# Optimization experiments

Measured on AMD Instinct MI355X. Metric: run time of the kernel, lower is better.

The kernel has to match this reference:

```python
import jax, jax.numpy as jnp
import numpy as np

B, H, S, D = 4, 8, 8192, 64


def setup_inputs() -> dict:
    key = jax.random.key(0)
    kq, kk, kv_, kqm, kkm = jax.random.split(key, 5)
    q = jax.random.normal(kq, (B, H, S, D), dtype=jnp.float32)
    k = jax.random.normal(kk, (B, H, S, D), dtype=jnp.float32)
    v = jax.random.normal(kv_, (B, H, S, D), dtype=jnp.float32)
    q_mask = jax.random.randint(kqm, (B, S), 0, 2).astype(jnp.bool_)
    kv_mask = jax.random.randint(kkm, (B, S), 0, 2).astype(jnp.bool_)
    return {"q": q, "k": k, "v": v, "q_mask": q_mask, "kv_mask": kv_mask}


def reference(q, k, v, q_mask, kv_mask):
    # Linear (kernelized) attention branch: feature map phi(x) = elu(x) + 1
    qe = jax.nn.elu(q) + 1.0
    ke = jax.nn.elu(k) + 1.0
    qm = q_mask.astype(q.dtype)[:, None, :, None]   # [B,1,S,1]
    km = kv_mask.astype(q.dtype)[:, None, :, None]
    qe = qe * qm
    ke = ke * km
    ve = v * km
    s = v.shape[2]
    # kv: [B,H,D,D] contraction over kv sequence
    kv = jnp.einsum('bhsd,bhsc->bhdc', ke, ve / s)
    # normalizer per query position: [B,H,L]
    div = 1.0 / (jnp.einsum('bhld,bhsd->bhl', qe, ke) + 1e-6)
    out = s * jnp.einsum('bhld,bhdc,bhl->bhlc', qe, kv, div)
    return out
```

## Files before the change

### kernel.cpp

```cpp
#include <hip/hip_runtime.h>


#define S_LEN 8192
#define NBH 32
#define KVSTRIDE 4160
#define NCHUNK 32
#define K3_XB 32

typedef __attribute__((ext_vector_type(4))) float f32x4;

__device__ __forceinline__ float elu1(float x) {
  return x > 0.0f ? (x + 1.0f) : __expf(x);
}

__global__ __launch_bounds__(256, 4) void k1_partial(
    const float* __restrict__ kin, const float* __restrict__ vin,
    const int* __restrict__ kv_mask, float* __restrict__ partials, int seg_rows) {
  __shared__ float ke_lds[64 * 64];
  __shared__ float ve_lds[64 * 64];
  const int tid = threadIdx.x;
  const int seg = blockIdx.x, bh = blockIdx.y, b = bh >> 3;
  const int rbase = seg * seg_rows;
  const int dg = tid >> 4, cg = tid & 15;
  const float* kbase = kin + (size_t)bh * S_LEN * 64;
  const float* vbase = vin + (size_t)bh * S_LEN * 64;
  const int* mbase = kv_mask + b * S_LEN;

  f32x4 kr[4], vr[4];
  float mr[4];
  float acc[4][4];
#pragma unroll
  for (int i = 0; i < 4; ++i)
#pragma unroll
    for (int j = 0; j < 4; ++j) acc[i][j] = 0.f;
  f32x4 ksump = {0.f, 0.f, 0.f, 0.f};

#define LOAD_T(r0_)                                                    \
  {                                                                    \
    const float* kp_ = kbase + (size_t)(r0_) * 64;                     \
    const float* vp_ = vbase + (size_t)(r0_) * 64;                     \
    _Pragma("unroll")                                                  \
    for (int i_ = 0; i_ < 4; ++i_) {                                   \
      int f_ = tid + 256 * i_;                                         \
      kr[i_] = *(const f32x4*)(kp_ + (size_t)f_ * 4);                  \
      vr[i_] = *(const f32x4*)(vp_ + (size_t)f_ * 4);                  \
      mr[i_] = mbase[(r0_) + dg + 16 * i_] ? 1.0f : 0.0f;              \
    }                                                                  \
  }

#define STORE_T()                                                      \
  {                                                                    \
    _Pragma("unroll")                                                  \
    for (int i_ = 0; i_ < 4; ++i_) {                                   \
      int row_ = dg + 16 * i_;                                         \
      float m_ = mr[i_];                                               \
      float mv_ = m_ * (1.0f / 8192.0f);                               \
      f32x4 ke4_, ve4_;                                                \
      _Pragma("unroll")                                                \
      for (int j_ = 0; j_ < 4; ++j_) {                                 \
        ke4_[j_] = elu1(kr[i_][j_]) * m_;                              \
        ve4_[j_] = vr[i_][j_] * mv_;                                   \
      }                                                                \
      ksump += ke4_;                                                   \
      *(f32x4*)&ke_lds[row_ * 64 + cg * 4] = ke4_;                     \
      *(f32x4*)&ve_lds[row_ * 64 + cg * 4] = ve4_;                     \
    }                                                                  \
  }

#define COMPUTE_T()                                                    \
  {                                                                    \
    _Pragma("unroll 4")                                                \
    for (int s_ = 0; s_ < 64; ++s_) {                                  \
      f32x4 kd_ = *(const f32x4*)&ke_lds[s_ * 64 + dg * 4];            \
      f32x4 vc_ = *(const f32x4*)&ve_lds[s_ * 64 + cg * 4];            \
      _Pragma("unroll")                                                \
      for (int i_ = 0; i_ < 4; ++i_)                                   \
        _Pragma("unroll")                                              \
        for (int j_ = 0; j_ < 4; ++j_)                                 \
          acc[i_][j_] = fmaf(kd_[i_], vc_[j_], acc[i_][j_]);           \
    }                                                                  \
  }

  const int ntiles = seg_rows >> 6;
  LOAD_T(rbase)
  for (int t = 0; t < ntiles; ++t) {
    if (t) __syncthreads();
    STORE_T()
    __syncthreads();
    if (t + 1 < ntiles) LOAD_T(rbase + (t + 1) * 64)
    COMPUTE_T()
  }

  float* p = partials + ((size_t)bh * gridDim.x + seg) * KVSTRIDE;
#pragma unroll
  for (int i = 0; i < 4; ++i) {
    f32x4 o;
#pragma unroll
    for (int j = 0; j < 4; ++j) o[j] = acc[i][j];
    *(f32x4*)&p[(dg * 4 + i) * 64 + cg * 4] = o;
  }
  __syncthreads();
  *(f32x4*)&ke_lds[tid * 4] = ksump;
  __syncthreads();
  if (tid < 64) {
    float s = 0.f;
#pragma unroll
    for (int g = 0; g < 16; ++g)
      s += ke_lds[(g * 16 + (tid >> 2)) * 4 + (tid & 3)];
    p[4096 + tid] = s;
  }
#undef LOAD_T
#undef STORE_T
#undef COMPUTE_T
}

__global__ __launch_bounds__(256) void k2_reduce(
    const float* __restrict__ partials, float* __restrict__ kvg, int nchunk) {
  const int idx = blockIdx.x * 256 + threadIdx.x;
  if (idx >= NBH * KVSTRIDE) return;
  const int bh = idx / KVSTRIDE;
  const int e = idx - bh * KVSTRIDE;
  const float* p = partials + (size_t)bh * nchunk * KVSTRIDE + e;
  float s0 = 0.f, s1 = 0.f, s2 = 0.f, s3 = 0.f;
  int c = 0;
  for (; c + 4 <= nchunk; c += 4) {
    s0 += p[(size_t)(c + 0) * KVSTRIDE];
    s1 += p[(size_t)(c + 1) * KVSTRIDE];
    s2 += p[(size_t)(c + 2) * KVSTRIDE];
    s3 += p[(size_t)(c + 3) * KVSTRIDE];
  }
  for (; c < nchunk; ++c) s0 += p[(size_t)c * KVSTRIDE];
  kvg[idx] = (s0 + s1) + (s2 + s3);
}

__global__ __launch_bounds__(256, 4) void k3_out(
    const float* __restrict__ qin, const int* __restrict__ q_mask,
    const float* __restrict__ kvg, float* __restrict__ out) {
  __shared__ float kv_lds[64 * 64];
  __shared__ float qe_lds[64 * 68];
  __shared__ float ks_lds[64];
  const int tid = threadIdx.x;
  const int xb = blockIdx.x, bh = blockIdx.y, b = bh >> 3;
  const int lg = tid >> 4, cg = tid & 15;
  const float* kvb = kvg + (size_t)bh * KVSTRIDE;
  const float* qb = qin + (size_t)bh * S_LEN * 64;
  const int* mb = q_mask + b * S_LEN;

#pragma unroll
  for (int i = 0; i < 4; ++i) {
    int f = tid + 256 * i;
    *(f32x4*)&kv_lds[f * 4] = *(const f32x4*)(kvb + (size_t)f * 4);
  }
  if (tid < 64) ks_lds[tid] = kvb[4096 + tid];

  f32x4 qr[4];
  float mr[4];

#define LOADQ(r0_)                                                     \
  {                                                                    \
    const float* qp_ = qb + (size_t)(r0_) * 64;                        \
    _Pragma("unroll")                                                  \
    for (int i_ = 0; i_ < 4; ++i_) {                                   \
      int f_ = tid + 256 * i_;                                         \
      qr[i_] = *(const f32x4*)(qp_ + (size_t)f_ * 4);                  \
      mr[i_] = mb[(r0_) + lg + 16 * i_] ? 1.0f : 0.0f;                 \
    }                                                                  \
  }

#define STOREQ()                                                       \
  {                                                                    \
    _Pragma("unroll")                                                  \
    for (int i_ = 0; i_ < 4; ++i_) {                                   \
      int row_ = lg + 16 * i_;                                         \
      float m_ = mr[i_];                                               \
      f32x4 qe_;                                                       \
      _Pragma("unroll")                                                \
      for (int j_ = 0; j_ < 4; ++j_) qe_[j_] = elu1(qr[i_][j_]) * m_;  \
      *(f32x4*)&qe_lds[row_ * 68 + cg * 4] = qe_;                      \
    }                                                                  \
  }

  const int c0 = xb * 4;
  LOADQ(c0 * 64)
  for (int t = 0; t < 4; ++t) {
    if (t) __syncthreads();
    STOREQ()
    __syncthreads();
    if (t + 1 < 4) LOADQ((c0 + t + 1) * 64)
    float acc[4][4];
    float den[4];
#pragma unroll
    for (int il = 0; il < 4; ++il) {
      den[il] = 0.f;
#pragma unroll
      for (int j = 0; j < 4; ++j) acc[il][j] = 0.f;
    }
#pragma unroll 8
    for (int d = 0; d < 64; d += 2) {
      float2 ksv = *(const float2*)&ks_lds[d];
      f32x4 kv0 = *(const f32x4*)&kv_lds[d * 64 + cg * 4];
      f32x4 kv1 = *(const f32x4*)&kv_lds[(d + 1) * 64 + cg * 4];
#pragma unroll
      for (int il = 0; il < 4; ++il) {
        float2 qv = *(const float2*)&qe_lds[(lg * 4 + il) * 68 + d];
        den[il] = fmaf(qv.x, ksv.x, fmaf(qv.y, ksv.y, den[il]));
#pragma unroll
        for (int j = 0; j < 4; ++j)
          acc[il][j] = fmaf(qv.x, kv0[j], fmaf(qv.y, kv1[j], acc[il][j]));
      }
    }
    const int r0 = (c0 + t) * 64;
#pragma unroll
    for (int il = 0; il < 4; ++il) {
      float inv = 8192.0f / (den[il] + 1e-6f);
      int row = r0 + lg * 4 + il;
      f32x4 o;
#pragma unroll
      for (int j = 0; j < 4; ++j) o[j] = acc[il][j] * inv;
      *(f32x4*)(out + ((size_t)bh * S_LEN + row) * 64 + cg * 4) = o;
    }
  }
#undef LOADQ
#undef STOREQ
}

extern "C" void kernel_launch(void* const* d_in, const int* in_sizes, int n_in,
                              void* d_out, int out_size, void* d_ws, size_t ws_size,
                              hipStream_t stream) {
  const float* q = (const float*)d_in[0];
  const float* k = (const float*)d_in[1];
  const float* v = (const float*)d_in[2];
  const int* qm = (const int*)d_in[3];
  const int* km = (const int*)d_in[4];
  float* out = (float*)d_out;

  int nchunk = NCHUNK;
  while (nchunk > 1) {
    size_t need = (size_t)NBH * nchunk * KVSTRIDE * 4 + (size_t)NBH * KVSTRIDE * 4;
    if (need <= ws_size) break;
    nchunk >>= 1;
  }
  float* partials = (float*)d_ws;
  float* kvg = partials + (size_t)NBH * nchunk * KVSTRIDE;
  int seg_rows = S_LEN / nchunk;

  k1_partial<<<dim3(nchunk, NBH), 256, 0, stream>>>(k, v, km, partials, seg_rows);
  int n_elem = NBH * KVSTRIDE;
  k2_reduce<<<dim3((n_elem + 255) / 256), 256, 0, stream>>>(partials, kvg, nchunk);
  k3_out<<<dim3(K3_XB, NBH), 256, 0, stream>>>(q, qm, kvg, out);
}
```

Baseline: 255.7 us.

## Use 8x8 register tiles with split-K reduction in k1 and k3

In k1 each thread now holds an 8x8 accumulator tile and each wave takes a quarter of the sequence rows. The four wave partials are then summed through LDS before the write. In k3 the launch changes to 128-row blocks with no inner loop; q is stored transposed in LDS, and two thread halves each take half of the D dimension, adding their results through LDS. The aim is to raise FMA-to-LDS-load intensity. The cost is more registers (launch bounds drop to 3 for k3), more LDS and extra reduction syncs.

```diff
diff --git a/kernel.cpp b/kernel.cpp
--- a/kernel.cpp
+++ b/kernel.cpp
@@ -5,7 +5,6 @@
 #define NBH 32
 #define KVSTRIDE 4160
 #define NCHUNK 32
-#define K3_XB 32
 
 typedef __attribute__((ext_vector_type(4))) float f32x4;
 
@@ -22,17 +21,20 @@
   const int seg = blockIdx.x, bh = blockIdx.y, b = bh >> 3;
   const int rbase = seg * seg_rows;
   const int dg = tid >> 4, cg = tid & 15;
+  const int w = tid >> 6, lane = tid & 63;
+  const int o8 = (lane >> 3) * 8;
+  const int c8 = (lane & 7) * 8;
   const float* kbase = kin + (size_t)bh * S_LEN * 64;
   const float* vbase = vin + (size_t)bh * S_LEN * 64;
   const int* mbase = kv_mask + b * S_LEN;
 
   f32x4 kr[4], vr[4];
   float mr[4];
-  float acc[4][4];
-#pragma unroll
-  for (int i = 0; i < 4; ++i)
-#pragma unroll
-    for (int j = 0; j < 4; ++j) acc[i][j] = 0.f;
+  float acc[8][8];
+#pragma unroll
+  for (int i = 0; i < 8; ++i)
+#pragma unroll
+    for (int j = 0; j < 8; ++j) acc[i][j] = 0.f;
   f32x4 ksump = {0.f, 0.f, 0.f, 0.f};
 
 #define LOAD_T(r0_)                                                    \
@@ -70,14 +72,21 @@
 #define COMPUTE_T()                                                    \
   {                                                                    \
     _Pragma("unroll 4")                                                \
-    for (int s_ = 0; s_ < 64; ++s_) {                                  \
-      f32x4 kd_ = *(const f32x4*)&ke_lds[s_ * 64 + dg * 4];            \
-      f32x4 vc_ = *(const f32x4*)&ve_lds[s_ * 64 + cg * 4];            \
+    for (int ss_ = 0; ss_ < 16; ++ss_) {                               \
+      const int s_ = (w << 4) + ss_;                                   \
+      f32x4 a0_ = *(const f32x4*)&ke_lds[s_ * 64 + o8];                \
+      f32x4 a1_ = *(const f32x4*)&ke_lds[s_ * 64 + o8 + 4];            \
+      f32x4 b0_ = *(const f32x4*)&ve_lds[s_ * 64 + c8];                \
+      f32x4 b1_ = *(const f32x4*)&ve_lds[s_ * 64 + c8 + 4];            \
       _Pragma("unroll")                                                \
       for (int i_ = 0; i_ < 4; ++i_)                                   \
         _Pragma("unroll")                                              \
-        for (int j_ = 0; j_ < 4; ++j_)                                 \
-          acc[i_][j_] = fmaf(kd_[i_], vc_[j_], acc[i_][j_]);           \
+        for (int j_ = 0; j_ < 4; ++j_) {                               \
+          acc[i_][j_]         = fmaf(a0_[i_], b0_[j_], acc[i_][j_]);   \
+          acc[i_][j_ + 4]     = fmaf(a0_[i_], b1_[j_], acc[i_][j_ + 4]); \
+          acc[i_ + 4][j_]     = fmaf(a1_[i_], b0_[j_], acc[i_ + 4][j_]); \
+          acc[i_ + 4][j_ + 4] = fmaf(a1_[i_], b1_[j_], acc[i_ + 4][j_ + 4]); \
+        }                                                              \
     }                                                                  \
   }
 
@@ -91,27 +100,67 @@
     COMPUTE_T()
   }
 
+#define ACC_W(buf_)                                                    \
+  {                                                                    \
+    _Pragma("unroll")                                                  \
+    for (int i_ = 0; i_ < 8; ++i_)                                     \
+      _Pragma("unroll")                                                \
+      for (int jq_ = 0; jq_ < 2; ++jq_) {                              \
+        f32x4 x_;                                                      \
+        _Pragma("unroll")                                              \
+        for (int j_ = 0; j_ < 4; ++j_) x_[j_] = acc[i_][jq_ * 4 + j_]; \
+        *(f32x4*)&buf_[(o8 + i_) * 64 + c8 + jq_ * 4] = x_;            \
+      }                                                                \
+  }
+#define ACC_A(buf_)                                                    \
+  {                                                                    \
+    _Pragma("unroll")                                                  \
+    for (int i_ = 0; i_ < 8; ++i_)                                     \
+      _Pragma("unroll")                                                \
+      for (int jq_ = 0; jq_ < 2; ++jq_) {                              \
+        f32x4 y_ = *(const f32x4*)&buf_[(o8 + i_) * 64 + c8 + jq_ * 4];\
+        _Pragma("unroll")                                              \
+        for (int j_ = 0; j_ < 4; ++j_) acc[i_][jq_ * 4 + j_] += y_[j_];\
+      }                                                                \
+  }
+
+  __syncthreads();
+  if (w == 2) ACC_W(ke_lds)
+  if (w == 3) ACC_W(ve_lds)
+  __syncthreads();
+  if (w == 0) ACC_A(ke_lds)
+  if (w == 1) ACC_A(ve_lds)
+  __syncthreads();
+  if (w == 1) ACC_W(ke_lds)
+  __syncthreads();
   float* p = partials + ((size_t)bh * gridDim.x + seg) * KVSTRIDE;
-#pragma unroll
-  for (int i = 0; i < 4; ++i) {
-    f32x4 o;
-#pragma unroll
-    for (int j = 0; j < 4; ++j) o[j] = acc[i][j];
-    *(f32x4*)&p[(dg * 4 + i) * 64 + cg * 4] = o;
-  }
-  __syncthreads();
-  *(f32x4*)&ke_lds[tid * 4] = ksump;
+  if (w == 0) {
+    ACC_A(ke_lds)
+#pragma unroll
+    for (int i = 0; i < 8; ++i)
+#pragma unroll
+      for (int jq = 0; jq < 2; ++jq) {
+        f32x4 o;
+#pragma unroll
+        for (int j = 0; j < 4; ++j) o[j] = acc[i][jq * 4 + j];
+        *(f32x4*)&p[(o8 + i) * 64 + c8 + jq * 4] = o;
+      }
+  }
+  __syncthreads();
+  *(f32x4*)&ve_lds[tid * 4] = ksump;
   __syncthreads();
   if (tid < 64) {
     float s = 0.f;
 #pragma unroll
     for (int g = 0; g < 16; ++g)
-      s += ke_lds[(g * 16 + (tid >> 2)) * 4 + (tid & 3)];
+      s += ve_lds[(g * 16 + (tid >> 2)) * 4 + (tid & 3)];
     p[4096 + tid] = s;
   }
 #undef LOAD_T
 #undef STORE_T
 #undef COMPUTE_T
+#undef ACC_W
+#undef ACC_A
 }
 
 __global__ __launch_bounds__(256) void k2_reduce(
@@ -133,18 +182,19 @@
   kvg[idx] = (s0 + s1) + (s2 + s3);
 }
 
-__global__ __launch_bounds__(256, 4) void k3_out(
+__global__ __launch_bounds__(256, 3) void k3_out(
     const float* __restrict__ qin, const int* __restrict__ q_mask,
     const float* __restrict__ kvg, float* __restrict__ out) {
+  __shared__ float qeT[64 * 132];
   __shared__ float kv_lds[64 * 64];
-  __shared__ float qe_lds[64 * 68];
+  __shared__ float den_lds[128];
   __shared__ float ks_lds[64];
   const int tid = threadIdx.x;
   const int xb = blockIdx.x, bh = blockIdx.y, b = bh >> 3;
-  const int lg = tid >> 4, cg = tid & 15;
+  const int r0 = xb * 128;
   const float* kvb = kvg + (size_t)bh * KVSTRIDE;
-  const float* qb = qin + (size_t)bh * S_LEN * 64;
-  const int* mb = q_mask + b * S_LEN;
+  const float* qb = qin + ((size_t)bh * S_LEN + r0) * 64;
+  const int* mb = q_mask + b * S_LEN + r0;
 
 #pragma unroll
   for (int i = 0; i < 4; ++i) {
@@ -153,75 +203,87 @@
   }
   if (tid < 64) ks_lds[tid] = kvb[4096 + tid];
 
-  f32x4 qr[4];
-  float mr[4];
-
-#define LOADQ(r0_)                                                     \
-  {                                                                    \
-    const float* qp_ = qb + (size_t)(r0_) * 64;                        \
-    _Pragma("unroll")                                                  \
-    for (int i_ = 0; i_ < 4; ++i_) {                                   \
-      int f_ = tid + 256 * i_;                                         \
-      qr[i_] = *(const f32x4*)(qp_ + (size_t)f_ * 4);                  \
-      mr[i_] = mb[(r0_) + lg + 16 * i_] ? 1.0f : 0.0f;                 \
-    }                                                                  \
-  }
-
-#define STOREQ()                                                       \
-  {                                                                    \
-    _Pragma("unroll")                                                  \
-    for (int i_ = 0; i_ < 4; ++i_) {                                   \
-      int row_ = lg + 16 * i_;                                         \
-      float m_ = mr[i_];                                               \
-      f32x4 qe_;                                                       \
-      _Pragma("unroll")                                                \
-      for (int j_ = 0; j_ < 4; ++j_) qe_[j_] = elu1(qr[i_][j_]) * m_;  \
-      *(f32x4*)&qe_lds[row_ * 68 + cg * 4] = qe_;                      \
-    }                                                                  \
-  }
-
-  const int c0 = xb * 4;
-  LOADQ(c0 * 64)
-  for (int t = 0; t < 4; ++t) {
-    if (t) __syncthreads();
-    STOREQ()
-    __syncthreads();
-    if (t + 1 < 4) LOADQ((c0 + t + 1) * 64)
-    float acc[4][4];
-    float den[4];
-#pragma unroll
-    for (int il = 0; il < 4; ++il) {
-      den[il] = 0.f;
-#pragma unroll
-      for (int j = 0; j < 4; ++j) acc[il][j] = 0.f;
-    }
-#pragma unroll 8
-    for (int d = 0; d < 64; d += 2) {
-      float2 ksv = *(const float2*)&ks_lds[d];
-      f32x4 kv0 = *(const f32x4*)&kv_lds[d * 64 + cg * 4];
-      f32x4 kv1 = *(const f32x4*)&kv_lds[(d + 1) * 64 + cg * 4];
-#pragma unroll
-      for (int il = 0; il < 4; ++il) {
-        float2 qv = *(const float2*)&qe_lds[(lg * 4 + il) * 68 + d];
-        den[il] = fmaf(qv.x, ksv.x, fmaf(qv.y, ksv.y, den[il]));
-#pragma unroll
-        for (int j = 0; j < 4; ++j)
-          acc[il][j] = fmaf(qv.x, kv0[j], fmaf(qv.y, kv1[j], acc[il][j]));
+#pragma unroll
+  for (int i = 0; i < 8; ++i) {
+    int f = tid + 256 * i;
+    int row = f >> 4, dq = f & 15;
+    float m = mb[row] ? 1.0f : 0.0f;
+    f32x4 qw = *(const f32x4*)(qb + (size_t)f * 4);
+#pragma unroll
+    for (int j = 0; j < 4; ++j)
+      qeT[(dq * 4 + j) * 132 + row] = elu1(qw[j]) * m;
+  }
+  __syncthreads();
+
+  const int g = tid >> 7;
+  const int idx = tid & 127;
+  const int l8 = (idx >> 3) * 8;
+  const int c8 = (idx & 7) * 8;
+  float acc[8][8];
+  float den[8];
+#pragma unroll
+  for (int i = 0; i < 8; ++i) {
+    den[i] = 0.f;
+#pragma unroll
+    for (int j = 0; j < 8; ++j) acc[i][j] = 0.f;
+  }
+  const int d0 = g * 32;
+#pragma unroll 4
+  for (int dd = 0; dd < 32; ++dd) {
+    const int d = d0 + dd;
+    f32x4 a0 = *(const f32x4*)&qeT[d * 132 + l8];
+    f32x4 a1 = *(const f32x4*)&qeT[d * 132 + l8 + 4];
+    f32x4 b0 = *(const f32x4*)&kv_lds[d * 64 + c8];
+    f32x4 b1 = *(const f32x4*)&kv_lds[d * 64 + c8 + 4];
+    float ks = ks_lds[d];
+#pragma unroll
+    for (int i = 0; i < 4; ++i) {
+      den[i]     = fmaf(a0[i], ks, den[i]);
+      den[i + 4] = fmaf(a1[i], ks, den[i + 4]);
+#pragma unroll
+      for (int j = 0; j < 4; ++j) {
+        acc[i][j]         = fmaf(a0[i], b0[j], acc[i][j]);
+        acc[i][j + 4]     = fmaf(a0[i], b1[j], acc[i][j + 4]);
+        acc[i + 4][j]     = fmaf(a1[i], b0[j], acc[i + 4][j]);
+        acc[i + 4][j + 4] = fmaf(a1[i], b1[j], acc[i + 4][j + 4]);
       }
     }
-    const int r0 = (c0 + t) * 64;
-#pragma unroll
-    for (int il = 0; il < 4; ++il) {
-      float inv = 8192.0f / (den[il] + 1e-6f);
-      int row = r0 + lg * 4 + il;
-      f32x4 o;
-#pragma unroll
-      for (int j = 0; j < 4; ++j) o[j] = acc[il][j] * inv;
-      *(f32x4*)(out + ((size_t)bh * S_LEN + row) * 64 + cg * 4) = o;
+  }
+
+  float* scratch = qeT;
+  __syncthreads();
+  if (g == 1) {
+#pragma unroll
+    for (int i = 0; i < 8; ++i)
+#pragma unroll
+      for (int jq = 0; jq < 2; ++jq) {
+        f32x4 x;
+#pragma unroll
+        for (int j = 0; j < 4; ++j) x[j] = acc[i][jq * 4 + j];
+        *(f32x4*)&scratch[(l8 + i) * 64 + c8 + jq * 4] = x;
+      }
+    if ((idx & 7) == 0) {
+#pragma unroll
+      for (int i = 0; i < 8; ++i) den_lds[l8 + i] = den[i];
     }
   }
-#undef LOADQ
-#undef STOREQ
+  __syncthreads();
+  if (g == 0) {
+#pragma unroll
+    for (int i = 0; i < 8; ++i) {
+      float dv = den[i] + den_lds[l8 + i];
+      float inv = 8192.0f / (dv + 1e-6f);
+      float* op = out + ((size_t)bh * S_LEN + r0 + l8 + i) * 64 + c8;
+#pragma unroll
+      for (int jq = 0; jq < 2; ++jq) {
+        f32x4 y = *(const f32x4*)&scratch[(l8 + i) * 64 + c8 + jq * 4];
+        f32x4 o;
+#pragma unroll
+        for (int j = 0; j < 4; ++j) o[j] = (acc[i][jq * 4 + j] + y[j]) * inv;
+        *(f32x4*)(op + jq * 4) = o;
+      }
+    }
+  }
 }
 
 extern "C" void kernel_launch(void* const* d_in, const int* in_sizes, int n_in,
@@ -247,5 +309,5 @@
   k1_partial<<<dim3(nchunk, NBH), 256, 0, stream>>>(k, v, km, partials, seg_rows);
   int n_elem = NBH * KVSTRIDE;
   k2_reduce<<<dim3((n_elem + 255) / 256), 256, 0, stream>>>(partials, kvg, nchunk);
-  k3_out<<<dim3(K3_XB, NBH), 256, 0, stream>>>(q, qm, kvg, out);
-}
+  k3_out<<<dim3(S_LEN / 128, NBH), 256, 0, stream>>>(q, qm, kvg, out);
+}
```

Measured after the change: 279.4 us. +9.3%, slower.
